# Kernel optimization log

Hardware: AMD Instinct MI355X
Metric: run time of the kernel (lower is better)

Reference implementation:

```python
import jax, jax.numpy as jnp
import numpy as np

N_NODES = 100000
N_EDGES = 1600000
D_IN = 128
D_OUT = 128


def setup_inputs() -> dict:
    key = jax.random.key(0)
    ks = jax.random.split(key, 7)
    x = jax.random.normal(ks[0], (N_NODES, D_IN), dtype=jnp.float32)
    h0 = jax.random.normal(ks[1], (N_NODES, D_IN), dtype=jnp.float32)
    adj_val = jax.random.uniform(ks[2], (N_EDGES,), dtype=jnp.float32)
    adj_src = jax.random.randint(ks[3], (N_EDGES,), 0, N_NODES, dtype=jnp.int32)
    adj_dst = jax.random.randint(ks[4], (N_EDGES,), 0, N_NODES, dtype=jnp.int32)
    stdv = 1.0 / np.sqrt(D_OUT)
    weight = jax.random.uniform(ks[5], (D_IN, D_OUT), dtype=jnp.float32, minval=-stdv, maxval=stdv)
    weight_r = jax.random.uniform(ks[6], (D_IN, D_OUT), dtype=jnp.float32, minval=-stdv, maxval=stdv)
    return {"x": x, "h0": h0, "adj_val": adj_val, "weight": weight,
            "weight_r": weight_r, "adj_src": adj_src, "adj_dst": adj_dst}


def reference(x, h0, adj_val, weight, weight_r, adj_src, adj_dst):
    # hi = spmm(adj, x): COO sparse matmul as weighted gather + segment-sum.
    msgs = adj_val[:, None] * x[adj_src]              # [E, D_IN]
    hi = jax.ops.segment_sum(msgs, adj_dst, num_segments=x.shape[0])  # [N, D_IN]
    # variant=False: no concat with h0. residual=True: + x @ weight_r.
    out = hi @ weight + x @ weight_r                   # [N, D_OUT]
    return out
```

## Files before the change

### kernel.cpp

```cpp
#include <hip/hip_runtime.h>
#include <hip/hip_fp16.h>


typedef __attribute__((ext_vector_type(8))) short bf16x8;
typedef __attribute__((ext_vector_type(4))) float f32x4;

#define BSH 8
#define CHUNK 4096
#define K2 18

__device__ __forceinline__ unsigned short f2b(float f) {
    unsigned u = __float_as_uint(f);
    return (unsigned short)((u + 0x7FFFu + ((u >> 16) & 1u)) >> 16);
}

__global__ __launch_bounds__(256) void wprep(const float* __restrict__ W,
                                             const float* __restrict__ Wr,
                                             unsigned short* __restrict__ Wt,
                                             unsigned short* __restrict__ Wrt,
                                             int* __restrict__ ccnt,
                                             int NBK) {
    int gid = blockIdx.x * 256 + threadIdx.x;
    if (gid < 16384) {
        int k = gid >> 7, n = gid & 127;
        Wt[(n << 7) + k]  = f2b(W[gid]);
        Wrt[(n << 7) + k] = f2b(Wr[gid]);
    }
    if (gid < NBK) ccnt[gid] = 0;
}

__global__ __launch_bounds__(512) void gemm_hist(const float* __restrict__ x,
                                                 const unsigned short* __restrict__ Wt,
                                                 const unsigned short* __restrict__ Wrt,
                                                 unsigned* __restrict__ z8u,
                                                 float* __restrict__ rowscale,
                                                 float* __restrict__ out, int N,
                                                 const int* __restrict__ dst,
                                                 int* __restrict__ ccnt,
                                                 int E, int NBK, int gemmBlocks) {
    __shared__ uint4 lw[4096];
    __shared__ int lh[512];

    if ((int)blockIdx.x >= gemmBlocks) {
        const int bb = (int)blockIdx.x - gemmBlocks;
        for (int i = threadIdx.x; i < NBK; i += 512) lh[i] = 0;
        __syncthreads();
        const int base = bb * CHUNK;
        #pragma unroll
        for (int i = 0; i < CHUNK / 512; ++i) {
            int e = base + i * 512 + threadIdx.x;
            if (e < E) atomicAdd(&lh[dst[e] >> BSH], 1);
        }
        __syncthreads();
        for (int i = threadIdx.x; i < NBK; i += 512)
            if (lh[i]) atomicAdd(&ccnt[i], lh[i]);
        return;
    }

    const int tid = threadIdx.x;
    const int wave = tid >> 6;
    const int lane = tid & 63;
    const int l15 = lane & 15;
    const int lhi = lane >> 4;

    const uint4* wtg = reinterpret_cast<const uint4*>(Wt);
    const uint4* wrg = reinterpret_cast<const uint4*>(Wrt);
    #pragma unroll
    for (int it = 0; it < 4; ++it) {
        int c = it * 512 + tid;
        int row = c >> 4, cc = c & 15;
        int sc = cc ^ (row & 7);
        lw[row * 16 + sc] = wtg[c];
        lw[2048 + row * 16 + sc] = wrg[c];
    }
    __syncthreads();

    const int rowBase = blockIdx.x * 256 + wave * 32;
    const int r0 = rowBase + l15;
    const int r1 = rowBase + 16 + l15;
    const size_t xo0 = (size_t)(r0 < N ? r0 : N - 1) * 128;
    const size_t xo1 = (size_t)(r1 < N ? r1 : N - 1) * 128;

    f32x4 accW[8][2], accR[8][2];
    #pragma unroll
    for (int fn = 0; fn < 8; ++fn) {
        accW[fn][0] = (f32x4)0.f; accW[fn][1] = (f32x4)0.f;
        accR[fn][0] = (f32x4)0.f; accR[fn][1] = (f32x4)0.f;
    }

    #pragma unroll
    for (int ks = 0; ks < 4; ++ks) {
        const int kb = ks * 32 + lhi * 8;
        float4 a0 = *reinterpret_cast<const float4*>(&x[xo0 + kb]);
        float4 b0 = *reinterpret_cast<const float4*>(&x[xo0 + kb + 4]);
        float4 a1 = *reinterpret_cast<const float4*>(&x[xo1 + kb]);
        float4 b1 = *reinterpret_cast<const float4*>(&x[xo1 + kb + 4]);
        union { bf16x8 v; unsigned u[4]; } xf0, xf1;
        xf0.u[0] = (unsigned)f2b(a0.x) | ((unsigned)f2b(a0.y) << 16);
        xf0.u[1] = (unsigned)f2b(a0.z) | ((unsigned)f2b(a0.w) << 16);
        xf0.u[2] = (unsigned)f2b(b0.x) | ((unsigned)f2b(b0.y) << 16);
        xf0.u[3] = (unsigned)f2b(b0.z) | ((unsigned)f2b(b0.w) << 16);
        xf1.u[0] = (unsigned)f2b(a1.x) | ((unsigned)f2b(a1.y) << 16);
        xf1.u[1] = (unsigned)f2b(a1.z) | ((unsigned)f2b(a1.w) << 16);
        xf1.u[2] = (unsigned)f2b(b1.x) | ((unsigned)f2b(b1.y) << 16);
        xf1.u[3] = (unsigned)f2b(b1.z) | ((unsigned)f2b(b1.w) << 16);

        const int sl = ks * 4 + lhi;
        #pragma unroll
        for (int fn = 0; fn < 8; ++fn) {
            int wrow = fn * 16 + l15;
            int idx = wrow * 16 + (sl ^ (wrow & 7));
            bf16x8 wf  = *reinterpret_cast<const bf16x8*>(&lw[idx]);
            bf16x8 wrf = *reinterpret_cast<const bf16x8*>(&lw[2048 + idx]);
            accW[fn][0] = __builtin_amdgcn_mfma_f32_16x16x32_bf16(wf,  xf0.v, accW[fn][0], 0, 0, 0);
            accW[fn][1] = __builtin_amdgcn_mfma_f32_16x16x32_bf16(wf,  xf1.v, accW[fn][1], 0, 0, 0);
            accR[fn][0] = __builtin_amdgcn_mfma_f32_16x16x32_bf16(wrf, xf0.v, accR[fn][0], 0, 0, 0);
            accR[fn][1] = __builtin_amdgcn_mfma_f32_16x16x32_bf16(wrf, xf1.v, accR[fn][1], 0, 0, 0);
        }
    }

    #pragma unroll
    for (int fr = 0; fr < 2; ++fr) {
        int row = rowBase + fr * 16 + l15;
        float m = 0.f;
        #pragma unroll
        for (int fn = 0; fn < 8; ++fn)
            #pragma unroll
            for (int j = 0; j < 4; ++j)
                m = fmaxf(m, fabsf(accW[fn][fr][j]));
        m = fmaxf(m, __shfl_xor(m, 16));
        m = fmaxf(m, __shfl_xor(m, 32));
        m = fmaxf(m, 1e-20f);
        const float qs = 127.0f / m;

        if (row >= N) continue;
        if (lhi == 0) rowscale[row] = m * (1.0f / 127.0f);
        #pragma unroll
        for (int fn = 0; fn < 8; ++fn) {
            int c = fn * 16 + lhi * 4;
            *reinterpret_cast<f32x4*>(&out[(size_t)row * 128 + c]) = accR[fn][fr];
            int q0 = (int)rintf(accW[fn][fr][0] * qs);
            int q1 = (int)rintf(accW[fn][fr][1] * qs);
            int q2 = (int)rintf(accW[fn][fr][2] * qs);
            int q3 = (int)rintf(accW[fn][fr][3] * qs);
            unsigned pq = (unsigned)(q0 & 255) | ((unsigned)(q1 & 255) << 8) |
                          ((unsigned)(q2 & 255) << 16) | ((unsigned)(q3 & 255) << 24);
            z8u[(size_t)row * 32 + fn * 4 + lhi] = pq;
        }
    }
}

__global__ __launch_bounds__(256) void scanc(const int* __restrict__ ccnt, int* __restrict__ coff,
                                             int* __restrict__ ccur, int NBK) {
    __shared__ int sh[256];
    const int t = threadIdx.x;
    const int i0 = t * 2;
    int c0 = (i0 < NBK) ? ccnt[i0] : 0;
    int c1 = (i0 + 1 < NBK) ? ccnt[i0 + 1] : 0;
    int s = c0 + c1;
    sh[t] = s;
    __syncthreads();
    #pragma unroll
    for (int d = 1; d < 256; d <<= 1) {
        int v = (t >= d) ? sh[t - d] : 0;
        __syncthreads();
        sh[t] += v;
        __syncthreads();
    }
    int ex = sh[t] - s;
    if (i0 < NBK) { coff[i0] = ex; ccur[i0] = ex; }
    if (i0 + 1 < NBK) { coff[i0 + 1] = ex + c0; ccur[i0 + 1] = ex + c0; }
}

__global__ __launch_bounds__(256) void binsort1(const float* __restrict__ val,
                                                const int* __restrict__ src,
                                                const int* __restrict__ dst,
                                                int* __restrict__ ccur,
                                                uint2* __restrict__ epk1, int E, int NBK) {
    __shared__ int lh[512];
    __shared__ int lbase[512];
    for (int i = threadIdx.x; i < NBK; i += 256) lh[i] = 0;
    __syncthreads();
    const int base = blockIdx.x * CHUNK;
    int rank[CHUNK / 256];
    int bk[CHUNK / 256];
    #pragma unroll
    for (int i = 0; i < CHUNK / 256; ++i) {
        int e = base + i * 256 + threadIdx.x;
        if (e < E) {
            int b = dst[e] >> BSH;
            bk[i] = b;
            rank[i] = atomicAdd(&lh[b], 1);
        } else bk[i] = -1;
    }
    __syncthreads();
    for (int i = threadIdx.x; i < NBK; i += 256)
        lbase[i] = lh[i] ? atomicAdd(&ccur[i], lh[i]) : 0;
    __syncthreads();
    #pragma unroll
    for (int i = 0; i < CHUNK / 256; ++i) {
        int e = base + i * 256 + threadIdx.x;
        if (e >= E) break;
        int p = lbase[bk[i]] + rank[i];
        __half hv = __float2half(val[e]);
        unsigned short hu;
        __builtin_memcpy(&hu, &hv, 2);
        epk1[p] = make_uint2((unsigned)src[e] | ((unsigned)(hu & 0x7FFFu) << 17),
                             (unsigned)dst[e]);
    }
}

__device__ __forceinline__ float h15f(unsigned h) {
    unsigned short u = (unsigned short)(h & 0x7FFFu);
    __half hv;
    __builtin_memcpy(&hv, &u, 2);
    return __half2float(hv);
}

__global__ __launch_bounds__(256) void binsort2(const uint2* __restrict__ epk1,
                                                const int* __restrict__ coff,
                                                const int* __restrict__ ccnt,
                                                const float* __restrict__ rowscale,
                                                unsigned* __restrict__ epk,
                                                int* __restrict__ off,
                                                int* __restrict__ cnt, int N) {
    __shared__ int lcnt[256];
    __shared__ int sh[256];
    __shared__ int lcur[256];
    const int b = blockIdx.x;
    const int s = coff[b];
    const int n = ccnt[b];
    const int t = threadIdx.x;
    const int gnode = (b << BSH) + t;

    lcnt[t] = 0;
    __syncthreads();

    uint2 q[K2];
    #pragma unroll
    for (int r = 0; r < K2; ++r) {
        int i = t + r * 256;
        if (i < n) {
            q[r] = epk1[s + i];
            atomicAdd(&lcnt[q[r].y & 255], 1);
        }
    }
    for (int i = t + K2 * 256; i < n; i += 256)
        atomicAdd(&lcnt[epk1[s + i].y & 255], 1);
    __syncthreads();

    int c = lcnt[t];
    sh[t] = c;
    __syncthreads();
    #pragma unroll
    for (int d = 1; d < 256; d <<= 1) {
        int v = (t >= d) ? sh[t - d] : 0;
        __syncthreads();
        sh[t] += v;
        __syncthreads();
    }
    int ex = sh[t] - c;
    lcur[t] = ex;
    if (gnode < N) {
        off[gnode] = s + ex;
        cnt[gnode] = c;
    }
    __syncthreads();

    #pragma unroll
    for (int r = 0; r < K2; ++r) {
        int i = t + r * 256;
        if (i < n) {
            unsigned srcv = q[r].x & 0x1FFFFu;
            float v = h15f(q[r].x >> 17) * rowscale[srcv];
            int p = s + atomicAdd(&lcur[q[r].y & 255], 1);
            epk[p] = (srcv << 15) | ((unsigned)f2b(v) & 0x7FFFu);
        }
    }
    for (int i = t + K2 * 256; i < n; i += 256) {
        uint2 v2 = epk1[s + i];
        unsigned srcv = v2.x & 0x1FFFFu;
        float v = h15f(v2.x >> 17) * rowscale[srcv];
        int p = s + atomicAdd(&lcur[v2.y & 255], 1);
        epk[p] = (srcv << 15) | ((unsigned)f2b(v) & 0x7FFFu);
    }
}

__global__ __launch_bounds__(256) void spmm_gather(const unsigned short* __restrict__ z8u,
                                                   const unsigned* __restrict__ epk,
                                                   const int* __restrict__ off,
                                                   const int* __restrict__ cnt,
                                                   float* __restrict__ out, int N) {
    const int lane = threadIdx.x & 63;
    const int node = (int)((blockIdx.x * (size_t)blockDim.x + threadIdx.x) >> 6);
    if (node >= N) return;
    const int base = __builtin_amdgcn_readfirstlane(off[node]);
    const int deg  = __builtin_amdgcn_readfirstlane(cnt[node]);
    const unsigned* __restrict__ ep = epk + base;

    float2 acc = *reinterpret_cast<const float2*>(&out[(size_t)node * 128 + lane * 2]);

    int j = 0;
    for (; j + 8 <= deg; j += 8) {
        unsigned p0 = ep[j + 0], p1 = ep[j + 1], p2 = ep[j + 2], p3 = ep[j + 3];
        unsigned p4 = ep[j + 4], p5 = ep[j + 5], p6 = ep[j + 6], p7 = ep[j + 7];
        unsigned short w0 = z8u[(size_t)(p0 >> 15) * 64 + lane];
        unsigned short w1 = z8u[(size_t)(p1 >> 15) * 64 + lane];
        unsigned short w2 = z8u[(size_t)(p2 >> 15) * 64 + lane];
        unsigned short w3 = z8u[(size_t)(p3 >> 15) * 64 + lane];
        unsigned short w4 = z8u[(size_t)(p4 >> 15) * 64 + lane];
        unsigned short w5 = z8u[(size_t)(p5 >> 15) * 64 + lane];
        unsigned short w6 = z8u[(size_t)(p6 >> 15) * 64 + lane];
        unsigned short w7 = z8u[(size_t)(p7 >> 15) * 64 + lane];
        float v0 = __uint_as_float((p0 & 0x7FFFu) << 16);
        float v1 = __uint_as_float((p1 & 0x7FFFu) << 16);
        float v2 = __uint_as_float((p2 & 0x7FFFu) << 16);
        float v3 = __uint_as_float((p3 & 0x7FFFu) << 16);
        float v4 = __uint_as_float((p4 & 0x7FFFu) << 16);
        float v5 = __uint_as_float((p5 & 0x7FFFu) << 16);
        float v6 = __uint_as_float((p6 & 0x7FFFu) << 16);
        float v7 = __uint_as_float((p7 & 0x7FFFu) << 16);
        acc.x = fmaf(v0, (float)(signed char)(w0 & 0xFF), acc.x);
        acc.y = fmaf(v0, (float)(signed char)(w0 >> 8), acc.y);
        acc.x = fmaf(v1, (float)(signed char)(w1 & 0xFF), acc.x);
        acc.y = fmaf(v1, (float)(signed char)(w1 >> 8), acc.y);
        acc.x = fmaf(v2, (float)(signed char)(w2 & 0xFF), acc.x);
        acc.y = fmaf(v2, (float)(signed char)(w2 >> 8), acc.y);
        acc.x = fmaf(v3, (float)(signed char)(w3 & 0xFF), acc.x);
        acc.y = fmaf(v3, (float)(signed char)(w3 >> 8), acc.y);
        acc.x = fmaf(v4, (float)(signed char)(w4 & 0xFF), acc.x);
        acc.y = fmaf(v4, (float)(signed char)(w4 >> 8), acc.y);
        acc.x = fmaf(v5, (float)(signed char)(w5 & 0xFF), acc.x);
        acc.y = fmaf(v5, (float)(signed char)(w5 >> 8), acc.y);
        acc.x = fmaf(v6, (float)(signed char)(w6 & 0xFF), acc.x);
        acc.y = fmaf(v6, (float)(signed char)(w6 >> 8), acc.y);
        acc.x = fmaf(v7, (float)(signed char)(w7 & 0xFF), acc.x);
        acc.y = fmaf(v7, (float)(signed char)(w7 >> 8), acc.y);
    }
    for (; j < deg; ++j) {
        unsigned p = ep[j];
        unsigned short wv = z8u[(size_t)(p >> 15) * 64 + lane];
        float v = __uint_as_float((p & 0x7FFFu) << 16);
        acc.x = fmaf(v, (float)(signed char)(wv & 0xFF), acc.x);
        acc.y = fmaf(v, (float)(signed char)(wv >> 8), acc.y);
    }
    *reinterpret_cast<float2*>(&out[(size_t)node * 128 + lane * 2]) = acc;
}

extern "C" void kernel_launch(void* const* d_in, const int* in_sizes, int n_in,
                              void* d_out, int out_size, void* d_ws, size_t ws_size,
                              hipStream_t stream) {
    const float* x    = (const float*)d_in[0];
    const float* aval = (const float*)d_in[2];
    const float* W    = (const float*)d_in[3];
    const float* Wr   = (const float*)d_in[4];
    const int*   asrc = (const int*)d_in[5];
    const int*   adst = (const int*)d_in[6];
    float* out = (float*)d_out;

    const int nx = in_sizes[0];
    const int N = nx / 128;
    const int E = in_sizes[2];
    const int NBK = (N + (1 << BSH) - 1) >> BSH;
    const int NB1 = (E + CHUNK - 1) / CHUNK;
    const int gemmBlocks = (N + 255) / 256;

    char* w = (char*)d_ws;
    uint2* epk1 = (uint2*)w;                  w += (size_t)E * 8;
    unsigned* z8 = (unsigned*)w;              w += (size_t)nx;
    float* rowscale = (float*)w;              w += (size_t)N * 4;
    unsigned short* Wt = (unsigned short*)w;  w += 16384 * 2;
    unsigned short* Wrt= (unsigned short*)w;  w += 16384 * 2;
    int* off    = (int*)w;  w += (size_t)N * 4;
    int* cnt    = (int*)w;  w += (size_t)N * 4;
    int* ccnt   = (int*)w;  w += 2048;
    int* coff   = (int*)w;  w += 2048;
    int* ccur   = (int*)w;  w += 2048;
    unsigned* epk = (unsigned*)w;  w += (size_t)E * 4;

    wprep<<<(16384 + 255) / 256, 256, 0, stream>>>(W, Wr, Wt, Wrt, ccnt, NBK);
    gemm_hist<<<gemmBlocks + NB1, 512, 0, stream>>>(x, Wt, Wrt, z8, rowscale, out, N,
                                                    adst, ccnt, E, NBK, gemmBlocks);
    scanc<<<1, 256, 0, stream>>>(ccnt, coff, ccur, NBK);
    binsort1<<<NB1, 256, 0, stream>>>(aval, asrc, adst, ccur, epk1, E, NBK);
    binsort2<<<NBK, 256, 0, stream>>>(epk1, coff, ccnt, rowscale, epk, off, cnt, N);
    spmm_gather<<<(int)(((size_t)N * 64 + 255) / 256), 256, 0, stream>>>(
        (const unsigned short*)z8, epk, off, cnt, out, N);
}
```

Measured before the change: 139.3 us.

## Restructure pipeline: fuse histogram with weight prep, scan into GEMM, shrink binsort traffic

Moves the destination histogram into the weight-prep kernel and the bucket scan into an extra block of the GEMM kernel. This removes the standalone scan launch and its serialization point. binsort1 now applies rowscale and packs the final bf16-scaled edge word directly, plus a separate byte array for the low destination bits. That cuts the intermediate from 8 to 5 bytes per edge and removes the scaled-value work from binsort2. It adds a memset launch, and binsort1 does a random rowscale gather, which costs some locality.

```diff
diff --git a/kernel.cpp b/kernel.cpp
--- a/kernel.cpp
+++ b/kernel.cpp
@@ -14,46 +14,63 @@
     return (unsigned short)((u + 0x7FFFu + ((u >> 16) & 1u)) >> 16);
 }
 
-__global__ __launch_bounds__(256) void wprep(const float* __restrict__ W,
-                                             const float* __restrict__ Wr,
-                                             unsigned short* __restrict__ Wt,
-                                             unsigned short* __restrict__ Wrt,
-                                             int* __restrict__ ccnt,
-                                             int NBK) {
-    int gid = blockIdx.x * 256 + threadIdx.x;
+__global__ __launch_bounds__(512) void prep_hist(const float* __restrict__ W,
+                                                 const float* __restrict__ Wr,
+                                                 unsigned short* __restrict__ Wt,
+                                                 unsigned short* __restrict__ Wrt,
+                                                 const int* __restrict__ dst,
+                                                 int* __restrict__ ccnt,
+                                                 int E, int NBK, int histBlocks) {
+    __shared__ int lh[512];
+    if ((int)blockIdx.x < histBlocks) {
+        for (int i = threadIdx.x; i < NBK; i += 512) lh[i] = 0;
+        __syncthreads();
+        const int base = blockIdx.x * CHUNK;
+        #pragma unroll
+        for (int i = 0; i < CHUNK / 512; ++i) {
+            int e = base + i * 512 + threadIdx.x;
+            if (e < E) atomicAdd(&lh[dst[e] >> BSH], 1);
+        }
+        __syncthreads();
+        for (int i = threadIdx.x; i < NBK; i += 512)
+            if (lh[i]) atomicAdd(&ccnt[i], lh[i]);
+        return;
+    }
+    int gid = ((int)blockIdx.x - histBlocks) * 512 + threadIdx.x;
     if (gid < 16384) {
         int k = gid >> 7, n = gid & 127;
         Wt[(n << 7) + k]  = f2b(W[gid]);
         Wrt[(n << 7) + k] = f2b(Wr[gid]);
     }
-    if (gid < NBK) ccnt[gid] = 0;
-}
-
-__global__ __launch_bounds__(512) void gemm_hist(const float* __restrict__ x,
+}
+
+__global__ __launch_bounds__(512) void gemm_scan(const float* __restrict__ x,
                                                  const unsigned short* __restrict__ Wt,
                                                  const unsigned short* __restrict__ Wrt,
                                                  unsigned* __restrict__ z8u,
                                                  float* __restrict__ rowscale,
                                                  float* __restrict__ out, int N,
-                                                 const int* __restrict__ dst,
-                                                 int* __restrict__ ccnt,
-                                                 int E, int NBK, int gemmBlocks) {
+                                                 const int* __restrict__ ccnt,
+                                                 int* __restrict__ coff,
+                                                 int* __restrict__ ccur,
+                                                 int NBK, int gemmBlocks) {
     __shared__ uint4 lw[4096];
-    __shared__ int lh[512];
+    __shared__ int sh2[512];
 
     if ((int)blockIdx.x >= gemmBlocks) {
-        const int bb = (int)blockIdx.x - gemmBlocks;
-        for (int i = threadIdx.x; i < NBK; i += 512) lh[i] = 0;
-        __syncthreads();
-        const int base = bb * CHUNK;
-        #pragma unroll
-        for (int i = 0; i < CHUNK / 512; ++i) {
-            int e = base + i * 512 + threadIdx.x;
-            if (e < E) atomicAdd(&lh[dst[e] >> BSH], 1);
-        }
-        __syncthreads();
-        for (int i = threadIdx.x; i < NBK; i += 512)
-            if (lh[i]) atomicAdd(&ccnt[i], lh[i]);
+        const int t = threadIdx.x;
+        int c = (t < NBK) ? ccnt[t] : 0;
+        sh2[t] = c;
+        __syncthreads();
+        #pragma unroll
+        for (int d = 1; d < 512; d <<= 1) {
+            int v = (t >= d) ? sh2[t - d] : 0;
+            __syncthreads();
+            sh2[t] += v;
+            __syncthreads();
+        }
+        int ex = sh2[t] - c;
+        if (t < NBK) { coff[t] = ex; ccur[t] = ex; }
         return;
     }
 
@@ -150,48 +167,29 @@
     }
 }
 
-__global__ __launch_bounds__(256) void scanc(const int* __restrict__ ccnt, int* __restrict__ coff,
-                                             int* __restrict__ ccur, int NBK) {
-    __shared__ int sh[256];
-    const int t = threadIdx.x;
-    const int i0 = t * 2;
-    int c0 = (i0 < NBK) ? ccnt[i0] : 0;
-    int c1 = (i0 + 1 < NBK) ? ccnt[i0 + 1] : 0;
-    int s = c0 + c1;
-    sh[t] = s;
-    __syncthreads();
-    #pragma unroll
-    for (int d = 1; d < 256; d <<= 1) {
-        int v = (t >= d) ? sh[t - d] : 0;
-        __syncthreads();
-        sh[t] += v;
-        __syncthreads();
-    }
-    int ex = sh[t] - s;
-    if (i0 < NBK) { coff[i0] = ex; ccur[i0] = ex; }
-    if (i0 + 1 < NBK) { coff[i0 + 1] = ex + c0; ccur[i0 + 1] = ex + c0; }
-}
-
 __global__ __launch_bounds__(256) void binsort1(const float* __restrict__ val,
                                                 const int* __restrict__ src,
                                                 const int* __restrict__ dst,
+                                                const float* __restrict__ rowscale,
                                                 int* __restrict__ ccur,
-                                                uint2* __restrict__ epk1, int E, int NBK) {
+                                                unsigned* __restrict__ epkA,
+                                                unsigned char* __restrict__ dstb,
+                                                int E, int NBK) {
     __shared__ int lh[512];
     __shared__ int lbase[512];
     for (int i = threadIdx.x; i < NBK; i += 256) lh[i] = 0;
     __syncthreads();
     const int base = blockIdx.x * CHUNK;
     int rank[CHUNK / 256];
-    int bk[CHUNK / 256];
+    int bkd8[CHUNK / 256];
     #pragma unroll
     for (int i = 0; i < CHUNK / 256; ++i) {
         int e = base + i * 256 + threadIdx.x;
         if (e < E) {
-            int b = dst[e] >> BSH;
-            bk[i] = b;
-            rank[i] = atomicAdd(&lh[b], 1);
-        } else bk[i] = -1;
+            int d = dst[e];
+            bkd8[i] = d;
+            rank[i] = atomicAdd(&lh[d >> BSH], 1);
+        } else bkd8[i] = -1;
     }
     __syncthreads();
     for (int i = threadIdx.x; i < NBK; i += 256)
@@ -201,26 +199,19 @@
     for (int i = 0; i < CHUNK / 256; ++i) {
         int e = base + i * 256 + threadIdx.x;
         if (e >= E) break;
-        int p = lbase[bk[i]] + rank[i];
-        __half hv = __float2half(val[e]);
-        unsigned short hu;
-        __builtin_memcpy(&hu, &hv, 2);
-        epk1[p] = make_uint2((unsigned)src[e] | ((unsigned)(hu & 0x7FFFu) << 17),
-                             (unsigned)dst[e]);
-    }
-}
-
-__device__ __forceinline__ float h15f(unsigned h) {
-    unsigned short u = (unsigned short)(h & 0x7FFFu);
-    __half hv;
-    __builtin_memcpy(&hv, &u, 2);
-    return __half2float(hv);
-}
-
-__global__ __launch_bounds__(256) void binsort2(const uint2* __restrict__ epk1,
+        int d = bkd8[i];
+        int p = lbase[d >> BSH] + rank[i];
+        unsigned s = (unsigned)src[e];
+        float v = val[e] * rowscale[s];
+        epkA[p] = (s << 15) | ((unsigned)f2b(v) & 0x7FFFu);
+        dstb[p] = (unsigned char)(d & 255);
+    }
+}
+
+__global__ __launch_bounds__(256) void binsort2(const unsigned* __restrict__ epkA,
+                                                const unsigned char* __restrict__ dstb,
                                                 const int* __restrict__ coff,
                                                 const int* __restrict__ ccnt,
-                                                const float* __restrict__ rowscale,
                                                 unsigned* __restrict__ epk,
                                                 int* __restrict__ off,
                                                 int* __restrict__ cnt, int N) {
@@ -236,17 +227,19 @@
     lcnt[t] = 0;
     __syncthreads();
 
-    uint2 q[K2];
+    unsigned q[K2];
+    int d8[K2];
     #pragma unroll
     for (int r = 0; r < K2; ++r) {
         int i = t + r * 256;
         if (i < n) {
-            q[r] = epk1[s + i];
-            atomicAdd(&lcnt[q[r].y & 255], 1);
+            q[r] = epkA[s + i];
+            d8[r] = dstb[s + i];
+            atomicAdd(&lcnt[d8[r]], 1);
         }
     }
     for (int i = t + K2 * 256; i < n; i += 256)
-        atomicAdd(&lcnt[epk1[s + i].y & 255], 1);
+        atomicAdd(&lcnt[dstb[s + i]], 1);
     __syncthreads();
 
     int c = lcnt[t];
@@ -271,18 +264,13 @@
     for (int r = 0; r < K2; ++r) {
         int i = t + r * 256;
         if (i < n) {
-            unsigned srcv = q[r].x & 0x1FFFFu;
-            float v = h15f(q[r].x >> 17) * rowscale[srcv];
-            int p = s + atomicAdd(&lcur[q[r].y & 255], 1);
-            epk[p] = (srcv << 15) | ((unsigned)f2b(v) & 0x7FFFu);
+            int p = s + atomicAdd(&lcur[d8[r]], 1);
+            epk[p] = q[r];
         }
     }
     for (int i = t + K2 * 256; i < n; i += 256) {
-        uint2 v2 = epk1[s + i];
-        unsigned srcv = v2.x & 0x1FFFFu;
-        float v = h15f(v2.x >> 17) * rowscale[srcv];
-        int p = s + atomicAdd(&lcur[v2.y & 255], 1);
-        epk[p] = (srcv << 15) | ((unsigned)f2b(v) & 0x7FFFu);
+        int p = s + atomicAdd(&lcur[dstb[s + i]], 1);
+        epk[p] = epkA[s + i];
     }
 }
 
@@ -364,9 +352,11 @@
     const int NBK = (N + (1 << BSH) - 1) >> BSH;
     const int NB1 = (E + CHUNK - 1) / CHUNK;
     const int gemmBlocks = (N + 255) / 256;
+    const int wprepBlocks = (16384 + 511) / 512;
 
     char* w = (char*)d_ws;
-    uint2* epk1 = (uint2*)w;                  w += (size_t)E * 8;
+    unsigned* epkA = (unsigned*)w;            w += (size_t)E * 4;
+    unsigned char* dstb = (unsigned char*)w;  w += ((size_t)E + 15) & ~15ull;
     unsigned* z8 = (unsigned*)w;              w += (size_t)nx;
     float* rowscale = (float*)w;              w += (size_t)N * 4;
     unsigned short* Wt = (unsigned short*)w;  w += 16384 * 2;
@@ -378,12 +368,12 @@
     int* ccur   = (int*)w;  w += 2048;
     unsigned* epk = (unsigned*)w;  w += (size_t)E * 4;
 
-    wprep<<<(16384 + 255) / 256, 256, 0, stream>>>(W, Wr, Wt, Wrt, ccnt, NBK);
-    gemm_hist<<<gemmBlocks + NB1, 512, 0, stream>>>(x, Wt, Wrt, z8, rowscale, out, N,
-                                                    adst, ccnt, E, NBK, gemmBlocks);
-    scanc<<<1, 256, 0, stream>>>(ccnt, coff, ccur, NBK);
-    binsort1<<<NB1, 256, 0, stream>>>(aval, asrc, adst, ccur, epk1, E, NBK);
-    binsort2<<<NBK, 256, 0, stream>>>(epk1, coff, ccnt, rowscale, epk, off, cnt, N);
+    hipMemsetAsync(ccnt, 0, (size_t)NBK * 4, stream);
+    prep_hist<<<NB1 + wprepBlocks, 512, 0, stream>>>(W, Wr, Wt, Wrt, adst, ccnt, E, NBK, NB1);
+    gemm_scan<<<gemmBlocks + 1, 512, 0, stream>>>(x, Wt, Wrt, z8, rowscale, out, N,
+                                                  ccnt, coff, ccur, NBK, gemmBlocks);
+    binsort1<<<NB1, 256, 0, stream>>>(aval, asrc, adst, rowscale, ccur, epkA, dstb, E, NBK);
+    binsort2<<<NBK, 256, 0, stream>>>(epkA, dstb, coff, ccnt, epk, off, cnt, N);
     spmm_gather<<<(int)(((size_t)N * 64 + 255) / 256), 256, 0, stream>>>(
         (const unsigned short*)z8, epk, off, cnt, out, N);
 }
```

New measurement: 155.8 us. 1.12x slower.

## Move histogram into weight-prep kernel and fold bucket scan into GEMM launch

Applied to the files above, without the earlier changes.

The destination-bucket histogram now runs in the same launch as the weight transpose/convert, and the prefix scan over bucket counts runs as an extra block of the GEMM kernel. This removes the standalone scan launch and keeps the scan's serial latency off the critical path. Counter zeroing moves to a memset, so the launch count stays the same. The scan now assumes at most 512 buckets, which holds for the current node count.

```diff
diff --git a/kernel.cpp b/kernel.cpp
--- a/kernel.cpp
+++ b/kernel.cpp
@@ -14,46 +14,63 @@
     return (unsigned short)((u + 0x7FFFu + ((u >> 16) & 1u)) >> 16);
 }
 
-__global__ __launch_bounds__(256) void wprep(const float* __restrict__ W,
-                                             const float* __restrict__ Wr,
-                                             unsigned short* __restrict__ Wt,
-                                             unsigned short* __restrict__ Wrt,
-                                             int* __restrict__ ccnt,
-                                             int NBK) {
-    int gid = blockIdx.x * 256 + threadIdx.x;
+__global__ __launch_bounds__(512) void prep_hist(const float* __restrict__ W,
+                                                 const float* __restrict__ Wr,
+                                                 unsigned short* __restrict__ Wt,
+                                                 unsigned short* __restrict__ Wrt,
+                                                 const int* __restrict__ dst,
+                                                 int* __restrict__ ccnt,
+                                                 int E, int NBK, int histBlocks) {
+    __shared__ int lh[512];
+    if ((int)blockIdx.x < histBlocks) {
+        for (int i = threadIdx.x; i < NBK; i += 512) lh[i] = 0;
+        __syncthreads();
+        const int base = blockIdx.x * CHUNK;
+        #pragma unroll
+        for (int i = 0; i < CHUNK / 512; ++i) {
+            int e = base + i * 512 + threadIdx.x;
+            if (e < E) atomicAdd(&lh[dst[e] >> BSH], 1);
+        }
+        __syncthreads();
+        for (int i = threadIdx.x; i < NBK; i += 512)
+            if (lh[i]) atomicAdd(&ccnt[i], lh[i]);
+        return;
+    }
+    int gid = ((int)blockIdx.x - histBlocks) * 512 + threadIdx.x;
     if (gid < 16384) {
         int k = gid >> 7, n = gid & 127;
         Wt[(n << 7) + k]  = f2b(W[gid]);
         Wrt[(n << 7) + k] = f2b(Wr[gid]);
     }
-    if (gid < NBK) ccnt[gid] = 0;
-}
-
-__global__ __launch_bounds__(512) void gemm_hist(const float* __restrict__ x,
+}
+
+__global__ __launch_bounds__(512) void gemm_scan(const float* __restrict__ x,
                                                  const unsigned short* __restrict__ Wt,
                                                  const unsigned short* __restrict__ Wrt,
                                                  unsigned* __restrict__ z8u,
                                                  float* __restrict__ rowscale,
                                                  float* __restrict__ out, int N,
-                                                 const int* __restrict__ dst,
-                                                 int* __restrict__ ccnt,
-                                                 int E, int NBK, int gemmBlocks) {
+                                                 const int* __restrict__ ccnt,
+                                                 int* __restrict__ coff,
+                                                 int* __restrict__ ccur,
+                                                 int NBK, int gemmBlocks) {
     __shared__ uint4 lw[4096];
-    __shared__ int lh[512];
+    __shared__ int sh2[512];
 
     if ((int)blockIdx.x >= gemmBlocks) {
-        const int bb = (int)blockIdx.x - gemmBlocks;
-        for (int i = threadIdx.x; i < NBK; i += 512) lh[i] = 0;
-        __syncthreads();
-        const int base = bb * CHUNK;
-        #pragma unroll
-        for (int i = 0; i < CHUNK / 512; ++i) {
-            int e = base + i * 512 + threadIdx.x;
-            if (e < E) atomicAdd(&lh[dst[e] >> BSH], 1);
-        }
-        __syncthreads();
-        for (int i = threadIdx.x; i < NBK; i += 512)
-            if (lh[i]) atomicAdd(&ccnt[i], lh[i]);
+        const int t = threadIdx.x;
+        int c = (t < NBK) ? ccnt[t] : 0;
+        sh2[t] = c;
+        __syncthreads();
+        #pragma unroll
+        for (int d = 1; d < 512; d <<= 1) {
+            int v = (t >= d) ? sh2[t - d] : 0;
+            __syncthreads();
+            sh2[t] += v;
+            __syncthreads();
+        }
+        int ex = sh2[t] - c;
+        if (t < NBK) { coff[t] = ex; ccur[t] = ex; }
         return;
     }
 
@@ -148,28 +165,6 @@
             z8u[(size_t)row * 32 + fn * 4 + lhi] = pq;
         }
     }
-}
-
-__global__ __launch_bounds__(256) void scanc(const int* __restrict__ ccnt, int* __restrict__ coff,
-                                             int* __restrict__ ccur, int NBK) {
-    __shared__ int sh[256];
-    const int t = threadIdx.x;
-    const int i0 = t * 2;
-    int c0 = (i0 < NBK) ? ccnt[i0] : 0;
-    int c1 = (i0 + 1 < NBK) ? ccnt[i0 + 1] : 0;
-    int s = c0 + c1;
-    sh[t] = s;
-    __syncthreads();
-    #pragma unroll
-    for (int d = 1; d < 256; d <<= 1) {
-        int v = (t >= d) ? sh[t - d] : 0;
-        __syncthreads();
-        sh[t] += v;
-        __syncthreads();
-    }
-    int ex = sh[t] - s;
-    if (i0 < NBK) { coff[i0] = ex; ccur[i0] = ex; }
-    if (i0 + 1 < NBK) { coff[i0 + 1] = ex + c0; ccur[i0 + 1] = ex + c0; }
 }
 
 __global__ __launch_bounds__(256) void binsort1(const float* __restrict__ val,
@@ -364,6 +359,7 @@
     const int NBK = (N + (1 << BSH) - 1) >> BSH;
     const int NB1 = (E + CHUNK - 1) / CHUNK;
     const int gemmBlocks = (N + 255) / 256;
+    const int wprepBlocks = (16384 + 511) / 512;
 
     char* w = (char*)d_ws;
     uint2* epk1 = (uint2*)w;                  w += (size_t)E * 8;
@@ -378,10 +374,10 @@
     int* ccur   = (int*)w;  w += 2048;
     unsigned* epk = (unsigned*)w;  w += (size_t)E * 4;
 
-    wprep<<<(16384 + 255) / 256, 256, 0, stream>>>(W, Wr, Wt, Wrt, ccnt, NBK);
-    gemm_hist<<<gemmBlocks + NB1, 512, 0, stream>>>(x, Wt, Wrt, z8, rowscale, out, N,
-                                                    adst, ccnt, E, NBK, gemmBlocks);
-    scanc<<<1, 256, 0, stream>>>(ccnt, coff, ccur, NBK);
+    hipMemsetAsync(ccnt, 0, (size_t)NBK * 4, stream);
+    prep_hist<<<NB1 + wprepBlocks, 512, 0, stream>>>(W, Wr, Wt, Wrt, adst, ccnt, E, NBK, NB1);
+    gemm_scan<<<gemmBlocks + 1, 512, 0, stream>>>(x, Wt, Wrt, z8, rowscale, out, N,
+                                                  ccnt, coff, ccur, NBK, gemmBlocks);
     binsort1<<<NB1, 256, 0, stream>>>(aval, asrc, adst, ccur, epk1, E, NBK);
     binsort2<<<NBK, 256, 0, stream>>>(epk1, coff, ccnt, rowscale, epk, off, cnt, N);
     spmm_gather<<<(int)(((size_t)N * 64 + 255) / 256), 256, 0, stream>>>(
```

Result: slower. 145.7 us (+4.6%).
